# Optimization experiments

Hardware: AMD Instinct MI355X
Metric: run time of the kernel (lower is better)

Reference implementation:

```python
import jax, jax.numpy as jnp
import numpy as np

B, S, D, H = 2, 2048, 1024, 16
DK = D // H

def setup_inputs() -> dict:
    key = jax.random.key(0)
    ks = jax.random.split(key, 11)
    scale = 1.0 / np.sqrt(D)
    inp = {
        'query': jax.random.normal(ks[0], (B, S, D), jnp.float32),
        'key':   jax.random.normal(ks[1], (B, S, D), jnp.float32),
        'value': jax.random.normal(ks[2], (B, S, D), jnp.float32),
        'wq': jax.random.normal(ks[3], (D, D), jnp.float32) * scale,
        'bq': jax.random.normal(ks[4], (D,), jnp.float32) * 0.01,
        'wk': jax.random.normal(ks[5], (D, D), jnp.float32) * scale,
        'bk': jax.random.normal(ks[6], (D,), jnp.float32) * 0.01,
        'wv': jax.random.normal(ks[7], (D, D), jnp.float32) * scale,
        'bv': jax.random.normal(ks[8], (D,), jnp.float32) * 0.01,
        'wo': jax.random.normal(ks[9], (D, D), jnp.float32) * scale,
        'bo': jax.random.normal(ks[10], (D,), jnp.float32) * 0.01,
    }
    return inp

def reference(query, key, value, wq, bq, wk, bk, wv, bv, wo, bo):
    nb = query.shape[0]
    # projections: torch nn.Linear computes x @ W^T + b; here weights stored as (in,out)
    def proj(x, w, b):
        return (x @ w + b).reshape(nb, -1, H, DK).transpose(0, 2, 1, 3)  # [B,H,S,dk]
    q = proj(query, wq, bq)
    k = proj(key, wk, bk)
    v = proj(value, wv, bv)
    scores = jnp.einsum('bhqd,bhkd->bhqk', q, k) / jnp.sqrt(jnp.float32(DK))
    p = jax.nn.softmax(scores, axis=-1)  # dropout p=0 (eval)
    x = jnp.einsum('bhqk,bhkd->bhqd', p, v)
    x = x.transpose(0, 2, 1, 3).reshape(nb, -1, H * DK)
    return x @ wo + bo
```

## Files before the change

kernel.cpp:

```cpp
#include <hip/hip_runtime.h>


typedef __attribute__((ext_vector_type(8))) __bf16 bf16x8;
typedef __attribute__((ext_vector_type(4))) __bf16 bf16x4;
typedef __attribute__((ext_vector_type(8))) float f32x8;
typedef __attribute__((ext_vector_type(4))) float f32x4;
typedef __attribute__((ext_vector_type(16))) float f32x16;
typedef unsigned uv2 __attribute__((ext_vector_type(2)));

#define MFMA16 __builtin_amdgcn_mfma_f32_16x16x32_bf16
#define MFMA32 __builtin_amdgcn_mfma_f32_32x32x16_bf16

union Bf8 { bf16x8 v; __bf16 e[8]; };

__device__ inline f32x4 zero4() { f32x4 z; z[0]=z[1]=z[2]=z[3]=0.f; return z; }
__device__ inline f32x16 zero16() {
    f32x16 z;
#pragma unroll
    for (int i = 0; i < 16; i++) z[i] = 0.f;
    return z;
}

__device__ inline float fast_exp2(float x) {
#if __has_builtin(__builtin_amdgcn_exp2f)
    return __builtin_amdgcn_exp2f(x);
#else
    return __expf(x * 0.6931471805599453f);
#endif
}

#if __has_builtin(__builtin_amdgcn_permlane32_swap)
#define HAVE_PLSWAP 1
#endif

__device__ inline void plswap32(unsigned &a, unsigned &b) {
#ifdef HAVE_PLSWAP
    uv2 r = __builtin_amdgcn_permlane32_swap(a, b, false, false);
    a = r[0]; b = r[1];
#else
    unsigned sa = __shfl_xor((int)a, 32), sb = __shfl_xor((int)b, 32);
    bool hi = (threadIdx.x & 32) != 0;
    unsigned na = hi ? sb : a;
    unsigned nb = hi ? b : sa;
    a = na; b = nb;
#endif
}

__device__ inline float red32_sum(float x) {
#ifdef HAVE_PLSWAP
    unsigned a = __float_as_uint(x), b = __float_as_uint(x);
    uv2 r = __builtin_amdgcn_permlane32_swap(a, b, false, false);
    return __uint_as_float(r[0]) + __uint_as_float(r[1]);
#else
    return x + __shfl_xor(x, 32);
#endif
}

__device__ inline unsigned pk2(float a, float b) {
    union { unsigned u; __bf16 e[2]; } r;
    r.e[0] = (__bf16)a; r.e[1] = (__bf16)b;
    return r.u;
}

__device__ inline void load_lds16(const void* g, void* l) {
    __builtin_amdgcn_global_load_lds(
        (const __attribute__((address_space(1))) unsigned int*)g,
        (__attribute__((address_space(3))) unsigned int*)l, 16, 0, 0);
}

__global__ __launch_bounds__(256) void prep_all(
        const float* __restrict__ w0, const float* __restrict__ w1,
        const float* __restrict__ w2, const float* __restrict__ w3,
        const float* __restrict__ x0, const float* __restrict__ x1,
        const float* __restrict__ x2,
        __bf16* __restrict__ wt, __bf16* __restrict__ d0,
        __bf16* __restrict__ d1, __bf16* __restrict__ d2) {
    const int z = blockIdx.z, t = threadIdx.x;
    if (z < 4) {
        const float* src = z == 0 ? w0 : z == 1 ? w1 : z == 2 ? w2 : w3;
        __bf16* dst = wt + (size_t)z * 1048576;
        __shared__ float tile[32][33];
        const int tc = t & 31, tr = t >> 5;
        const int r0 = blockIdx.y * 32, c0 = blockIdx.x * 32;
#pragma unroll
        for (int i = 0; i < 4; i++) {
            int r = tr + i * 8;
            tile[r][tc] = src[(size_t)(r0 + r) * 1024 + c0 + tc];
        }
        __syncthreads();
#pragma unroll
        for (int i = 0; i < 4; i++) {
            int r = tr + i * 8;
            dst[(size_t)(c0 + r) * 1024 + r0 + tc] = (__bf16)tile[tc][r];
        }
    } else {
        const float* src = z == 4 ? x0 : z == 5 ? x1 : x2;
        __bf16* dst = z == 4 ? d0 : z == 5 ? d1 : d2;
        int bid = blockIdx.y * 32 + blockIdx.x;
        size_t g = ((size_t)bid * 256 + t) * 16;
#pragma unroll
        for (int h = 0; h < 2; h++) {
            f32x8 a = *(const f32x8*)&src[g + h * 8];
            Bf8 tmp;
#pragma unroll
            for (int j = 0; j < 8; j++) tmp.e[j] = (__bf16)a[j];
            *(bf16x8*)&dst[g + h * 8] = tmp.v;
        }
    }
}

template <int MODE, typename OutT>
__device__ inline void gemm_fast_core(__bf16* __restrict__ smem,
                                      const __bf16* __restrict__ A,
                                      const __bf16* __restrict__ Bt,
                                      const float* __restrict__ bias,
                                      OutT* __restrict__ out, float scale) {
    __bf16* As = smem;
    __bf16* Bs = smem + 8192;
    const int t = threadIdx.x;
    const int wave = t >> 6, lane = t & 63, lm = lane & 15, quad = lane >> 4;
    const int m0 = blockIdx.y * 128, n0 = blockIdx.x * 128;
    const int wm = (wave >> 1) * 64, wn = (wave & 1) * 64;

    f32x4 acc[4][4];
#pragma unroll
    for (int i = 0; i < 4; i++)
#pragma unroll
        for (int j = 0; j < 4; j++) acc[i][j] = zero4();

    for (int k0 = 0; k0 < 1024; k0 += 64) {
#pragma unroll
        for (int i = 0; i < 4; i++) {
            int s = i * 256 + t;
            int row = s >> 3, cb = (s & 7) ^ (row & 7);
            size_t goff = (size_t)row * 1024 + k0 + cb * 8;
            load_lds16(&A[(size_t)m0 * 1024 + goff],
                       &As[(size_t)(i * 256 + wave * 64) * 8]);
            load_lds16(&Bt[(size_t)n0 * 1024 + goff],
                       &Bs[(size_t)(i * 256 + wave * 64) * 8]);
        }
        __syncthreads();
#pragma unroll
        for (int ks = 0; ks < 2; ks++) {
            bf16x8 af[4], bfr[4];
#pragma unroll
            for (int mt = 0; mt < 4; mt++)
                af[mt] = *(const bf16x8*)&As[(wm + mt * 16 + lm) * 64 +
                                             (((ks * 4 + quad) ^ (lm & 7)) * 8)];
#pragma unroll
            for (int nt = 0; nt < 4; nt++)
                bfr[nt] = *(const bf16x8*)&Bs[(wn + nt * 16 + lm) * 64 +
                                              (((ks * 4 + quad) ^ (lm & 7)) * 8)];
#pragma unroll
            for (int mt = 0; mt < 4; mt++)
#pragma unroll
                for (int nt = 0; nt < 4; nt++)
                    acc[mt][nt] = MFMA16(af[mt], bfr[nt], acc[mt][nt], 0, 0, 0);
        }
        __syncthreads();
    }

    float bv4[4];
#pragma unroll
    for (int nt = 0; nt < 4; nt++) bv4[nt] = bias[n0 + wn + nt * 16 + lm];

    if (MODE == 2) {
#pragma unroll
        for (int mt = 0; mt < 4; mt++)
#pragma unroll
            for (int r = 0; r < 4; r++) {
                int rr = wm + mt * 16 + quad * 4 + r;
#pragma unroll
                for (int nt = 0; nt < 4; nt++) {
                    int c = wn + nt * 16 + lm;
                    smem[c * 128 + (rr ^ (8 * (c & 15)))] =
                        (__bf16)((acc[mt][nt][r] + bv4[nt]) * scale);
                }
            }
        __syncthreads();
        const int b = m0 >> 11;
#pragma unroll
        for (int it = 0; it < 8; it++) {
            int g = it * 256 + t;
            int c = g >> 4, gr = g & 15;
            bf16x8 v = *(const bf16x8*)&smem[c * 128 + ((gr * 8) ^ (8 * (c & 15)))];
            int col = n0 + c, hh = col >> 6, dk = col & 63;
            int sglob = (m0 & 2047) + gr * 8;
            size_t idx = (size_t)(b * 16 + hh) * 131072 + (size_t)dk * 2048 + sglob;
            *(bf16x8*)&out[idx] = v;
        }
    } else {
#pragma unroll
        for (int mt = 0; mt < 4; mt++) {
#pragma unroll
            for (int r = 0; r < 4; r++) {
                int row = m0 + wm + mt * 16 + quad * 4 + r;
#pragma unroll
                for (int nt = 0; nt < 4; nt++) {
                    int col = n0 + wn + nt * 16 + lm;
                    float val = (acc[mt][nt][r] + bv4[nt]) * scale;
                    size_t idx;
                    if (MODE == 0) {
                        idx = (size_t)row * 1024 + col;
                    } else {
                        int b = row >> 11, s = row & 2047, hh = col >> 6, dk = col & 63;
                        idx = (size_t)(b * 16 + hh) * 131072 + (size_t)s * 64 + dk;
                    }
                    out[idx] = (OutT)val;
                }
            }
        }
    }
}

__global__ __launch_bounds__(256) void proj_fast3(
        const __bf16* __restrict__ xq, const __bf16* __restrict__ xk,
        const __bf16* __restrict__ xv, const __bf16* __restrict__ WT,
        const float* __restrict__ bq, const float* __restrict__ bk,
        const float* __restrict__ bv,
        __bf16* __restrict__ Q, __bf16* __restrict__ K, __bf16* __restrict__ Vt) {
    __shared__ __bf16 smem[16384];
    int z = blockIdx.z;
    if (z == 0)
        gemm_fast_core<1, __bf16>(smem, xq, WT, bq, Q, 0.18033688f);
    else if (z == 1)
        gemm_fast_core<1, __bf16>(smem, xk, WT + 1048576, bk, K, 1.f);
    else
        gemm_fast_core<2, __bf16>(smem, xv, WT + 2097152, bv, Vt, 1.f);
}

__global__ __launch_bounds__(256) void out_proj_fast64(
        const __bf16* __restrict__ A, const __bf16* __restrict__ Bt,
        const float* __restrict__ bias, float* __restrict__ out) {
    __shared__ __bf16 As[8192];
    __shared__ __bf16 Bs[4096];
    const int t = threadIdx.x;
    const int wave = t >> 6, lane = t & 63, lm = lane & 15, quad = lane >> 4;
    const int m0 = blockIdx.y * 128, n0 = blockIdx.x * 64;
    const int wm = (wave >> 1) * 64, wn = (wave & 1) * 32;

    f32x4 acc[4][2];
#pragma unroll
    for (int i = 0; i < 4; i++) { acc[i][0] = zero4(); acc[i][1] = zero4(); }

    for (int k0 = 0; k0 < 1024; k0 += 64) {
#pragma unroll
        for (int i = 0; i < 4; i++) {
            int s = i * 256 + t;
            int row = s >> 3, cb = (s & 7) ^ (row & 7);
            load_lds16(&A[(size_t)(m0 + row) * 1024 + k0 + cb * 8],
                       &As[(size_t)(i * 256 + wave * 64) * 8]);
            if (i < 2)
                load_lds16(&Bt[(size_t)(n0 + row) * 1024 + k0 + cb * 8],
                           &Bs[(size_t)(i * 256 + wave * 64) * 8]);
        }
        __syncthreads();
#pragma unroll
        for (int ks = 0; ks < 2; ks++) {
            bf16x8 af[4], bfr[2];
#pragma unroll
            for (int mt = 0; mt < 4; mt++)
                af[mt] = *(const bf16x8*)&As[(wm + mt * 16 + lm) * 64 +
                                             (((ks * 4 + quad) ^ (lm & 7)) * 8)];
#pragma unroll
            for (int nt = 0; nt < 2; nt++)
                bfr[nt] = *(const bf16x8*)&Bs[(wn + nt * 16 + lm) * 64 +
                                              (((ks * 4 + quad) ^ (lm & 7)) * 8)];
#pragma unroll
            for (int mt = 0; mt < 4; mt++)
#pragma unroll
                for (int nt = 0; nt < 2; nt++)
                    acc[mt][nt] = MFMA16(af[mt], bfr[nt], acc[mt][nt], 0, 0, 0);
        }
        __syncthreads();
    }

    float bv2[2];
#pragma unroll
    for (int nt = 0; nt < 2; nt++) bv2[nt] = bias[n0 + wn + nt * 16 + lm];

#pragma unroll
    for (int mt = 0; mt < 4; mt++)
#pragma unroll
        for (int r = 0; r < 4; r++) {
            int row = m0 + wm + mt * 16 + quad * 4 + r;
#pragma unroll
            for (int nt = 0; nt < 2; nt++) {
                int col = n0 + wn + nt * 16 + lm;
                out[(size_t)row * 1024 + col] = acc[mt][nt][r] + bv2[nt];
            }
        }
}

__global__ __launch_bounds__(256, 2) void attn_kernel(
        const __bf16* __restrict__ Q, const __bf16* __restrict__ K,
        const __bf16* __restrict__ Vt, __bf16* __restrict__ O) {
    __shared__ __bf16 smem[32768];
    const int t = threadIdx.x;
    const int wave = t >> 6, lane = t & 63;
    const int l31 = lane & 31, h = lane >> 5;
    const int q0 = blockIdx.x * 128;
    const int bh = blockIdx.y;
    const size_t base = (size_t)bh * 131072;

    bf16x8 bq[4];
    {
        int qrow = q0 + wave * 32 + l31;
#pragma unroll
        for (int kst = 0; kst < 4; kst++)
            bq[kst] = *(const bf16x8*)&Q[base + (size_t)qrow * 64 + kst * 16 + h * 8];
    }

    unsigned fo[4];
#pragma unroll
    for (int k = 0; k < 4; k++)
        fo[k] = (unsigned)(l31 * 64 +
                (((k * 2 + h) ^ (l31 & 7) ^ ((l31 >> 3) & 3)) * 8));

    const unsigned vrow = (unsigned)(l31 * 128);
    const unsigned hy = (unsigned)(h ^ (l31 & 15));

    unsigned dst4[4], ksrc4[4], vsrc4[4];
#pragma unroll
    for (int i = 0; i < 4; i++) {
        int s = i * 256 + t;
        int kr = s >> 3, kcb = (s & 7) ^ (kr & 7) ^ ((kr >> 3) & 3);
        int vr = s >> 4, vcb = (s & 15) ^ (vr & 15);
        dst4[i] = (unsigned)((i * 256 + wave * 64) * 8);
        ksrc4[i] = (unsigned)(kr * 64 + kcb * 8);
        vsrc4[i] = (unsigned)(vr * 2048 + vcb * 8);
    }

    float m_run = 0.f, l_run = 0.f;
    bool rescaled = false;
    f32x16 o_acc[2];
    o_acc[0] = zero16();
    o_acc[1] = zero16();
    bf16x8 bp[8];

    auto stageK = [&](int buf, int kv0) {
#pragma unroll
        for (int i = 0; i < 4; i++)
            load_lds16(&K[base + (size_t)kv0 * 64 + ksrc4[i]],
                       &smem[buf * 8192 + dst4[i]]);
    };
    auto stageV = [&](int buf, int kv0) {
#pragma unroll
        for (int i = 0; i < 4; i++)
            load_lds16(&Vt[base + (size_t)kv0 + vsrc4[i]],
                       &smem[16384 + buf * 8192 + dst4[i]]);
    };

    stageK(0, 0);
    __syncthreads();

    auto body = [&](int it, int cur) {
        const int kv0 = it * 128;
        if (it < 15) stageK(cur ^ 1, kv0 + 128);
        stageV(cur, kv0);

        f32x16 sc[4];
#pragma unroll
        for (int m = 0; m < 4; m++) sc[m] = zero16();
        __builtin_amdgcn_s_setprio(1);
#pragma unroll
        for (int mtk = 0; mtk < 4; mtk++)
#pragma unroll
            for (int kst = 0; kst < 4; kst++) {
                bf16x8 ak = *(const bf16x8*)&smem[cur * 8192 + mtk * 2048 + fo[kst]];
                sc[mtk] = MFMA32(ak, bq[kst], sc[mtk], 0, 0, 0);
            }
        if (it > 0) {
#pragma unroll
            for (int kb = 0; kb < 8; kb++)
#pragma unroll
                for (int mtd = 0; mtd < 2; mtd++) {
                    bf16x8 av = *(const bf16x8*)&smem[16384 + (cur ^ 1) * 8192 +
                                                      mtd * 4096 + vrow +
                                                      (((kb * 2) ^ hy) * 8)];
                    o_acc[mtd] = MFMA32(av, bp[kb], o_acc[mtd], 0, 0, 0);
                }
        }
        __builtin_amdgcn_s_setprio(0);

        if (!rescaled) {
#pragma unroll
            for (int m = 0; m < 4; m++)
#pragma unroll
                for (int r = 0; r < 16; r++) sc[m][r] = fast_exp2(sc[m][r]);
        } else {
#pragma unroll
            for (int m = 0; m < 4; m++)
#pragma unroll
                for (int r = 0; r < 16; r++) sc[m][r] = fast_exp2(sc[m][r] - m_run);
        }
        float tr[16];
#pragma unroll
        for (int i = 0; i < 16; i++)
            tr[i] = (sc[0][i] + sc[1][i]) + (sc[2][i] + sc[3][i]);
#pragma unroll
        for (int st = 8; st >= 1; st >>= 1)
#pragma unroll
            for (int i = 0; i < st; i++) tr[i] += tr[i + st];
        float su = tr[0];
        if (!__all(su <= 1048576.f)) {
            float pm[16];
#pragma unroll
            for (int i = 0; i < 16; i++)
                pm[i] = fmaxf(fmaxf(sc[0][i], sc[1][i]), fmaxf(sc[2][i], sc[3][i]));
#pragma unroll
            for (int st = 8; st >= 1; st >>= 1)
#pragma unroll
                for (int i = 0; i < st; i++) pm[i] = fmaxf(pm[i], pm[i + st]);
            float pmax = pm[0];
#ifdef HAVE_PLSWAP
            {
                unsigned a = __float_as_uint(pmax), b = a;
                uv2 rr = __builtin_amdgcn_permlane32_swap(a, b, false, false);
                pmax = fmaxf(__uint_as_float(rr[0]), __uint_as_float(rr[1]));
            }
#else
            pmax = fmaxf(pmax, __shfl_xor(pmax, 32));
#endif
            float alpha = 1.f / pmax;
            m_run += __log2f(pmax);
            rescaled = true;
#pragma unroll
            for (int m = 0; m < 4; m++)
#pragma unroll
                for (int r = 0; r < 16; r++) sc[m][r] *= alpha;
#pragma unroll
            for (int mtd = 0; mtd < 2; mtd++)
#pragma unroll
                for (int r = 0; r < 16; r++) o_acc[mtd][r] *= alpha;
            l_run *= alpha;
            su *= alpha;
        }
        l_run += su;

#pragma unroll
        for (int kb = 0; kb < 8; kb++) {
            const int mt = kb >> 1, g = (kb & 1) * 2;
            unsigned A0 = pk2(sc[mt][g * 4 + 0], sc[mt][g * 4 + 1]);
            unsigned A1 = pk2(sc[mt][g * 4 + 2], sc[mt][g * 4 + 3]);
            unsigned B0 = pk2(sc[mt][g * 4 + 4], sc[mt][g * 4 + 5]);
            unsigned B1 = pk2(sc[mt][g * 4 + 6], sc[mt][g * 4 + 7]);
            plswap32(A0, B0);
            plswap32(A1, B1);
            union { unsigned u[4]; bf16x8 v; } bb;
            bb.u[0] = A0; bb.u[1] = A1; bb.u[2] = B0; bb.u[3] = B1;
            bp[kb] = bb.v;
        }

        __syncthreads();
    };

    for (int it = 0; it < 16; it += 2) {
        body(it, 0);
        body(it + 1, 1);
    }

    {
        __builtin_amdgcn_s_setprio(1);
#pragma unroll
        for (int kb = 0; kb < 8; kb++)
#pragma unroll
            for (int mtd = 0; mtd < 2; mtd++) {
                bf16x8 av = *(const bf16x8*)&smem[16384 + 8192 + mtd * 4096 + vrow +
                                                  (((kb * 2) ^ hy) * 8)];
                o_acc[mtd] = MFMA32(av, bp[kb], o_acc[mtd], 0, 0, 0);
            }
        __builtin_amdgcn_s_setprio(0);
    }
    __syncthreads();

    {
        float inv = 1.f / red32_sum(l_run);
        __bf16* Osc = &smem[wave * 2176];
#pragma unroll
        for (int mtd = 0; mtd < 2; mtd++)
#pragma unroll
            for (int c = 0; c < 4; c++) {
                bf16x4 pk4;
#pragma unroll
                for (int r2 = 0; r2 < 4; r2++)
                    pk4[r2] = (__bf16)(o_acc[mtd][c * 4 + r2] * inv);
                *(bf16x4*)&Osc[l31 * 68 + mtd * 32 + c * 8 + h * 4] = pk4;
            }
        __asm__ volatile("" ::: "memory");
        const int b = bh >> 4, hh = bh & 15;
        int ql = lane >> 1, half = lane & 1;
        int srow = q0 + wave * 32 + ql;
#pragma unroll
        for (int j = 0; j < 4; j++) {
            bf16x8 v = *(const bf16x8*)&Osc[ql * 68 + half * 32 + j * 8];
            *(bf16x8*)&O[(size_t)(b * 2048 + srow) * 1024 + hh * 64 + half * 32 + j * 8] = v;
        }
    }
}

extern "C" void kernel_launch(void* const* d_in, const int* in_sizes, int n_in,
                              void* d_out, int out_size, void* d_ws, size_t ws_size,
                              hipStream_t stream) {
    if (ws_size < ((size_t)40 << 20)) return;

    const float* query = (const float*)d_in[0];
    const float* key_  = (const float*)d_in[1];
    const float* value = (const float*)d_in[2];
    const float* wq = (const float*)d_in[3];
    const float* bq = (const float*)d_in[4];
    const float* wk = (const float*)d_in[5];
    const float* bk = (const float*)d_in[6];
    const float* wv = (const float*)d_in[7];
    const float* bv = (const float*)d_in[8];
    const float* wo = (const float*)d_in[9];
    const float* bo = (const float*)d_in[10];
    float* out = (float*)d_out;

    char* ws = (char*)d_ws;
    __bf16* WT  = (__bf16*)(ws);
    __bf16* Qw  = (__bf16*)(ws + ((size_t)8  << 20));
    __bf16* Kw  = (__bf16*)(ws + ((size_t)16 << 20));
    __bf16* Vtw = (__bf16*)(ws + ((size_t)24 << 20));
    __bf16* Ow  = (__bf16*)(ws + ((size_t)32 << 20));

    __bf16* Xq = Ow;
    __bf16* Xk = (__bf16*)d_out;
    __bf16* Xv = (__bf16*)d_out + 4194304;

    prep_all<<<dim3(32, 32, 7), dim3(256), 0, stream>>>(
        wq, wk, wv, wo, query, key_, value, WT, Xq, Xk, Xv);
    proj_fast3<<<dim3(8, 32, 3), dim3(256), 0, stream>>>(
        Xq, Xk, Xv, WT, bq, bk, bv, Qw, Kw, Vtw);
    attn_kernel<<<dim3(16, 32), dim3(256), 0, stream>>>(Qw, Kw, Vtw, Ow);
    out_proj_fast64<<<dim3(16, 32), dim3(256), 0, stream>>>(
        Ow, WT + 3 * 1048576, bo, out);
}
```

Baseline: 224.6 us.

## Remap block indices for L2/XCD locality and move bf16 packing before row-sum

Block indices in the projection, output-projection and attention kernels are remapped so that groups of eight consecutive blocks share output columns or heads. This is meant to improve L2 reuse across the MI355X's chiplets, which receive blocks round-robin. Separately, the attention loop now packs exp values to bf16 before the row-sum reduction, so the packing/permlane work can overlap with the sum. When the overflow-rescale branch fires, the packing is redone.

```diff
diff --git a/kernel.cpp b/kernel.cpp
--- a/kernel.cpp
+++ b/kernel.cpp
@@ -114,12 +114,12 @@
                                       const __bf16* __restrict__ A,
                                       const __bf16* __restrict__ Bt,
                                       const float* __restrict__ bias,
-                                      OutT* __restrict__ out, float scale) {
+                                      OutT* __restrict__ out, float scale,
+                                      int m0, int n0) {
     __bf16* As = smem;
     __bf16* Bs = smem + 8192;
     const int t = threadIdx.x;
     const int wave = t >> 6, lane = t & 63, lm = lane & 15, quad = lane >> 4;
-    const int m0 = blockIdx.y * 128, n0 = blockIdx.x * 128;
     const int wm = (wave >> 1) * 64, wn = (wave & 1) * 64;
 
     f32x4 acc[4][4];
@@ -220,13 +220,16 @@
         const float* __restrict__ bv,
         __bf16* __restrict__ Q, __bf16* __restrict__ K, __bf16* __restrict__ Vt) {
     __shared__ __bf16 smem[16384];
+    const int lz = blockIdx.y * 8 + blockIdx.x;
+    const int m0 = ((lz & 7) + 8 * (lz >> 6)) * 128;
+    const int n0 = ((lz >> 3) & 7) * 128;
     int z = blockIdx.z;
     if (z == 0)
-        gemm_fast_core<1, __bf16>(smem, xq, WT, bq, Q, 0.18033688f);
+        gemm_fast_core<1, __bf16>(smem, xq, WT, bq, Q, 0.18033688f, m0, n0);
     else if (z == 1)
-        gemm_fast_core<1, __bf16>(smem, xk, WT + 1048576, bk, K, 1.f);
+        gemm_fast_core<1, __bf16>(smem, xk, WT + 1048576, bk, K, 1.f, m0, n0);
     else
-        gemm_fast_core<2, __bf16>(smem, xv, WT + 2097152, bv, Vt, 1.f);
+        gemm_fast_core<2, __bf16>(smem, xv, WT + 2097152, bv, Vt, 1.f, m0, n0);
 }
 
 __global__ __launch_bounds__(256) void out_proj_fast64(
@@ -236,7 +239,9 @@
     __shared__ __bf16 Bs[4096];
     const int t = threadIdx.x;
     const int wave = t >> 6, lane = t & 63, lm = lane & 15, quad = lane >> 4;
-    const int m0 = blockIdx.y * 128, n0 = blockIdx.x * 64;
+    const int l = blockIdx.y * 16 + blockIdx.x;
+    const int m0 = ((l & 7) + 8 * (l >> 7)) * 128;
+    const int n0 = ((l >> 3) & 15) * 64;
     const int wm = (wave >> 1) * 64, wn = (wave & 1) * 32;
 
     f32x4 acc[4][2];
@@ -299,8 +304,9 @@
     const int t = threadIdx.x;
     const int wave = t >> 6, lane = t & 63;
     const int l31 = lane & 31, h = lane >> 5;
-    const int q0 = blockIdx.x * 128;
-    const int bh = blockIdx.y;
+    const int l = blockIdx.y * 16 + blockIdx.x;
+    const int bh = (l & 7) + 8 * (l >> 7);
+    const int q0 = ((l >> 3) & 15) * 128;
     const size_t base = (size_t)bh * 131072;
 
     bf16x8 bq[4];
@@ -394,49 +400,6 @@
 #pragma unroll
                 for (int r = 0; r < 16; r++) sc[m][r] = fast_exp2(sc[m][r] - m_run);
         }
-        float tr[16];
-#pragma unroll
-        for (int i = 0; i < 16; i++)
-            tr[i] = (sc[0][i] + sc[1][i]) + (sc[2][i] + sc[3][i]);
-#pragma unroll
-        for (int st = 8; st >= 1; st >>= 1)
-#pragma unroll
-            for (int i = 0; i < st; i++) tr[i] += tr[i + st];
-        float su = tr[0];
-        if (!__all(su <= 1048576.f)) {
-            float pm[16];
-#pragma unroll
-            for (int i = 0; i < 16; i++)
-                pm[i] = fmaxf(fmaxf(sc[0][i], sc[1][i]), fmaxf(sc[2][i], sc[3][i]));
-#pragma unroll
-            for (int st = 8; st >= 1; st >>= 1)
-#pragma unroll
-                for (int i = 0; i < st; i++) pm[i] = fmaxf(pm[i], pm[i + st]);
-            float pmax = pm[0];
-#ifdef HAVE_PLSWAP
-            {
-                unsigned a = __float_as_uint(pmax), b = a;
-                uv2 rr = __builtin_amdgcn_permlane32_swap(a, b, false, false);
-                pmax = fmaxf(__uint_as_float(rr[0]), __uint_as_float(rr[1]));
-            }
-#else
-            pmax = fmaxf(pmax, __shfl_xor(pmax, 32));
-#endif
-            float alpha = 1.f / pmax;
-            m_run += __log2f(pmax);
-            rescaled = true;
-#pragma unroll
-            for (int m = 0; m < 4; m++)
-#pragma unroll
-                for (int r = 0; r < 16; r++) sc[m][r] *= alpha;
-#pragma unroll
-            for (int mtd = 0; mtd < 2; mtd++)
-#pragma unroll
-                for (int r = 0; r < 16; r++) o_acc[mtd][r] *= alpha;
-            l_run *= alpha;
-            su *= alpha;
-        }
-        l_run += su;
 
 #pragma unroll
         for (int kb = 0; kb < 8; kb++) {
@@ -451,6 +414,63 @@
             bb.u[0] = A0; bb.u[1] = A1; bb.u[2] = B0; bb.u[3] = B1;
             bp[kb] = bb.v;
         }
+
+        float tr[16];
+#pragma unroll
+        for (int i = 0; i < 16; i++)
+            tr[i] = (sc[0][i] + sc[1][i]) + (sc[2][i] + sc[3][i]);
+#pragma unroll
+        for (int st = 8; st >= 1; st >>= 1)
+#pragma unroll
+            for (int i = 0; i < st; i++) tr[i] += tr[i + st];
+        float su = tr[0];
+        if (!__all(su <= 1048576.f)) {
+            float pm[16];
+#pragma unroll
+            for (int i = 0; i < 16; i++)
+                pm[i] = fmaxf(fmaxf(sc[0][i], sc[1][i]), fmaxf(sc[2][i], sc[3][i]));
+#pragma unroll
+            for (int st = 8; st >= 1; st >>= 1)
+#pragma unroll
+                for (int i = 0; i < st; i++) pm[i] = fmaxf(pm[i], pm[i + st]);
+            float pmax = pm[0];
+#ifdef HAVE_PLSWAP
+            {
+                unsigned a = __float_as_uint(pmax), b = a;
+                uv2 rr = __builtin_amdgcn_permlane32_swap(a, b, false, false);
+                pmax = fmaxf(__uint_as_float(rr[0]), __uint_as_float(rr[1]));
+            }
+#else
+            pmax = fmaxf(pmax, __shfl_xor(pmax, 32));
+#endif
+            float alpha = 1.f / pmax;
+            m_run += __log2f(pmax);
+            rescaled = true;
+#pragma unroll
+            for (int m = 0; m < 4; m++)
+#pragma unroll
+                for (int r = 0; r < 16; r++) sc[m][r] *= alpha;
+#pragma unroll
+            for (int kb = 0; kb < 8; kb++) {
+                const int mt = kb >> 1, g = (kb & 1) * 2;
+                unsigned A0 = pk2(sc[mt][g * 4 + 0], sc[mt][g * 4 + 1]);
+                unsigned A1 = pk2(sc[mt][g * 4 + 2], sc[mt][g * 4 + 3]);
+                unsigned B0 = pk2(sc[mt][g * 4 + 4], sc[mt][g * 4 + 5]);
+                unsigned B1 = pk2(sc[mt][g * 4 + 6], sc[mt][g * 4 + 7]);
+                plswap32(A0, B0);
+                plswap32(A1, B1);
+                union { unsigned u[4]; bf16x8 v; } bb;
+                bb.u[0] = A0; bb.u[1] = A1; bb.u[2] = B0; bb.u[3] = B1;
+                bp[kb] = bb.v;
+            }
+#pragma unroll
+            for (int mtd = 0; mtd < 2; mtd++)
+#pragma unroll
+                for (int r = 0; r < 16; r++) o_acc[mtd][r] *= alpha;
+            l_run *= alpha;
+            su *= alpha;
+        }
+        l_run += su;
 
         __syncthreads();
     };
```

Result: slower. 243.0 us (+8.2%).
